# Performance work log

Hardware: AMD Instinct MI355X
Metric: run time of the kernel (lower is better)

## Reference

```python
import jax, jax.numpy as jnp
import numpy as np

KN = 2048       # 12*N spatio-temporal tokens
B = 4           # batch
D_MODEL = 512
N_HEADS = 8
HEAD_DIM = D_MODEL // N_HEADS
FACTOR = 5
U_PART = min(FACTOR * int(np.ceil(np.log(KN))), KN)  # sample_k == n_top == 40


def setup_inputs() -> dict:
    rng = jax.random.key(0)
    ks = jax.random.split(rng, 12)
    d = D_MODEL
    wscale = 1.0 / np.sqrt(d)  # xavier-ish init scale
    return {
        "query": jax.random.normal(ks[0], (KN, B, d), jnp.float32),
        "key": jax.random.normal(ks[1], (KN, B, d), jnp.float32),
        "value": jax.random.normal(ks[2], (KN, B, d), jnp.float32),
        "index_sample": jax.random.randint(ks[3], (KN, U_PART), 0, KN),
        "Wq": jax.random.normal(ks[4], (d, d), jnp.float32) * wscale,
        "bq": jnp.zeros((d,), jnp.float32),
        "Wk": jax.random.normal(ks[5], (d, d), jnp.float32) * wscale,
        "bk": jnp.zeros((d,), jnp.float32),
        "Wv": jax.random.normal(ks[6], (d, d), jnp.float32) * wscale,
        "bv": jnp.zeros((d,), jnp.float32),
        "Wo": jax.random.normal(ks[7], (d, d), jnp.float32) * wscale,
        "bo": jnp.zeros((d,), jnp.float32),
    }


def reference(query, key, value, index_sample, Wq, bq, Wk, bk, Wv, bv, Wo, bo):
    kN, Bb, d = query.shape
    H, E = N_HEADS, HEAD_DIM
    scaling = E ** -0.5

    # projections (torch Linear: x @ W.T + b); q is scaled before reshaping
    q = (query @ Wq.T + bq) * scaling
    k = key @ Wk.T + bk
    v = value @ Wv.T + bv

    # [kN, B, d] -> [B, H, kN, E]
    def to_bhne(x):
        return x.reshape(kN, Bb, H, E).transpose(1, 2, 0, 3)

    Q, K, V = to_bhne(q), to_bhne(k), to_bhne(v)

    # ProbSparse: sample U_PART keys per query row (shared index table)
    K_samp = K[:, :, index_sample, :]                       # [B,H,kN,S,E]
    QK_samp = jnp.einsum('bhne,bhnse->bhns', Q, K_samp)      # [B,H,kN,S]
    # sparsity measure M = max - mean(over full kN, as in source)
    M = QK_samp.max(axis=-1) - QK_samp.sum(axis=-1) / kN     # [B,H,kN]
    _, M_top = jax.lax.top_k(M, U_PART)                      # [B,H,S]

    # reduced queries attend over ALL keys
    Q_red = jnp.take_along_axis(Q, M_top[..., None], axis=2)  # [B,H,S,E]
    scores = jnp.einsum('bhse,bhne->bhsn', Q_red, K)          # [B,H,S,kN]
    attn = jax.nn.softmax(scores, axis=-1)
    upd = jnp.einsum('bhsn,bhne->bhse', attn, V)              # [B,H,S,E]

    # initial context = mean(V) broadcast; scatter-update the top rows
    ctx = jnp.broadcast_to(V.mean(axis=2, keepdims=True), V.shape)  # [B,H,kN,E]
    bi = jnp.arange(Bb)[:, None, None]
    hi = jnp.arange(H)[None, :, None]
    ctx = ctx.at[bi, hi, M_top].set(upd)

    out = ctx.transpose(0, 2, 1, 3).reshape(Bb, kN, d) @ Wo.T + bo  # [B,kN,d]
    return out
```

## Files before the change

kernel.cpp:

```cpp
#include <hip/hip_runtime.h>
#include <hip/hip_bf16.h>

#define KN 2048
#define BB 4
#define DM 512
#define NH 8
#define HE 64
#define UP 40
#define NBH 32
#define NROWS 8192
#define MiB(x) ((size_t)(x) << 20)

typedef __attribute__((ext_vector_type(8))) short short8;
typedef __attribute__((ext_vector_type(4))) float f32x4;

__device__ __forceinline__ ushort f2bf(float x) {
  unsigned u = __float_as_uint(x);
  unsigned r = (u + 0x7FFFu + ((u >> 16) & 1u)) >> 16;
  return (ushort)r;
}
__device__ __forceinline__ float bf2f(ushort h) {
  return __uint_as_float((unsigned)h << 16);
}

__global__ __launch_bounds__(256) void wsplit3_kernel(
    const float* __restrict__ W0, const float* __restrict__ W1,
    const float* __restrict__ W2, ushort* __restrict__ Wh,
    ushort* __restrict__ Wl) {
  const int which = blockIdx.x >> 9;
  const float* W = (which == 0) ? W0 : (which == 1) ? W1 : W2;
  size_t base = (size_t)which * 262144;
  int i = ((blockIdx.x & 511) * 256 + threadIdx.x) * 2;
  float2 v = *(const float2*)(W + i);
  ushort h0 = f2bf(v.x), h1 = f2bf(v.y);
  ushort l0 = f2bf(v.x - bf2f(h0)), l1 = f2bf(v.y - bf2f(h1));
  *(ushort2*)(Wh + base + i) = make_ushort2(h0, h1);
  *(ushort2*)(Wl + base + i) = make_ushort2(l0, l1);
}

#define APAD 40
__global__ __launch_bounds__(256) void gemm3_mfma(
    const float* __restrict__ A0, const float* __restrict__ A1,
    const float* __restrict__ A2,
    const ushort* __restrict__ Wh3, const ushort* __restrict__ Wl3,
    const float* __restrict__ bq, const float* __restrict__ bk,
    const float* __restrict__ bv, float* __restrict__ QKV) {
  __shared__ ushort AsH[128 * APAD];
  __shared__ ushort AsL[128 * APAD];
  __shared__ ushort WsH[128 * APAD];
  __shared__ ushort WsL[128 * APAD];

  const int which = blockIdx.x >> 8;
  const int local = blockIdx.x & 255;
  const int mt = (local & 7) * 8 + ((local >> 3) & 7);
  const int ot = local >> 6;
  const int m0 = mt * 128, o0 = ot * 128;

  const float* A = (which == 0) ? A0 : (which == 1) ? A1 : A2;
  const ushort* Wh = Wh3 + (size_t)which * 262144;
  const ushort* Wl = Wl3 + (size_t)which * 262144;
  const float* bias = (which == 0) ? bq : (which == 1) ? bk : bv;
  float* C = QKV + (size_t)which * 8192 * 512;
  const float scale = (which == 0) ? 0.125f : 1.0f;

  const int tid = threadIdx.x;
  const int w = tid >> 6, lane = tid & 63;
  const int wr = w >> 1, wc = w & 1;
  const int fr = lane & 15;
  const int kc = lane >> 4;

  f32x4 acc[4][4];
#pragma unroll
  for (int i = 0; i < 4; ++i)
#pragma unroll
    for (int j = 0; j < 4; ++j)
#pragma unroll
      for (int r = 0; r < 4; ++r) acc[i][j][r] = 0.f;

  const int r0 = tid >> 2, kq0 = (tid & 3) * 8;
  const int r1 = (tid + 256) >> 2, kq1 = ((tid + 256) & 3) * 8;
  const int lo0 = r0 * APAD + kq0, lo1 = r1 * APAD + kq1;

  for (int k0 = 0; k0 < 512; k0 += 32) {
#pragma unroll
    for (int i = 0; i < 4; ++i) {
      int c = tid + i * 256;
      int row = c >> 3, q = c & 7;
      float4 v = *(const float4*)(A + (size_t)(m0 + row) * 512 + k0 + q * 4);
      ushort h0 = f2bf(v.x), h1 = f2bf(v.y), h2 = f2bf(v.z), h3 = f2bf(v.w);
      ushort l0 = f2bf(v.x - bf2f(h0)), l1 = f2bf(v.y - bf2f(h1));
      ushort l2 = f2bf(v.z - bf2f(h2)), l3 = f2bf(v.w - bf2f(h3));
      *(ushort4*)(AsH + row * APAD + q * 4) = make_ushort4(h0, h1, h2, h3);
      *(ushort4*)(AsL + row * APAD + q * 4) = make_ushort4(l0, l1, l2, l3);
    }
    {
      size_t gw0 = (size_t)(o0 + r0) * 512 + k0 + kq0;
      size_t gw1 = (size_t)(o0 + r1) * 512 + k0 + kq1;
      *(short8*)(WsH + lo0) = *(const short8*)(Wh + gw0);
      *(short8*)(WsL + lo0) = *(const short8*)(Wl + gw0);
      *(short8*)(WsH + lo1) = *(const short8*)(Wh + gw1);
      *(short8*)(WsL + lo1) = *(const short8*)(Wl + gw1);
    }
    __syncthreads();

    short8 ah[4], al[4], bh[4], bl[4];
#pragma unroll
    for (int i = 0; i < 4; ++i) {
      int off = (wr * 64 + i * 16 + fr) * APAD + kc * 8;
      ah[i] = *(const short8*)(AsH + off);
      al[i] = *(const short8*)(AsL + off);
    }
#pragma unroll
    for (int j = 0; j < 4; ++j) {
      int off = (wc * 64 + j * 16 + fr) * APAD + kc * 8;
      bh[j] = *(const short8*)(WsH + off);
      bl[j] = *(const short8*)(WsL + off);
    }
#pragma unroll
    for (int i = 0; i < 4; ++i)
#pragma unroll
      for (int j = 0; j < 4; ++j) {
        acc[i][j] = __builtin_amdgcn_mfma_f32_16x16x32_bf16(
            ah[i], bh[j], acc[i][j], 0, 0, 0);
        acc[i][j] = __builtin_amdgcn_mfma_f32_16x16x32_bf16(
            ah[i], bl[j], acc[i][j], 0, 0, 0);
        acc[i][j] = __builtin_amdgcn_mfma_f32_16x16x32_bf16(
            al[i], bh[j], acc[i][j], 0, 0, 0);
      }
    __syncthreads();
  }

#pragma unroll
  for (int i = 0; i < 4; ++i)
#pragma unroll
    for (int j = 0; j < 4; ++j)
#pragma unroll
      for (int r = 0; r < 4; ++r) {
        int m = m0 + wr * 64 + i * 16 + (lane >> 4) * 4 + r;
        int o = o0 + wc * 64 + j * 16 + fr;
        C[(size_t)m * 512 + o] = (acc[i][j][r] + bias[o]) * scale;
      }
}

__global__ __launch_bounds__(256) void transposeK_kernel(
    const float* __restrict__ K, float* __restrict__ Kt) {
  const int bh = blockIdx.x & 31;
  const int nt = blockIdx.x >> 5;
  const int b = bh >> 3, h = bh & 7;
  const int n0 = nt * 128;
  const int tid = threadIdx.x;
  __shared__ float T[128][65];

#pragma unroll
  for (int i = 0; i < 8; ++i) {
    int flat = tid + i * 256;
    int r = flat >> 4;
    int c4 = flat & 15;
    float4 v = *(const float4*)(K + (((size_t)(n0 + r) * 4 + b) * 8 + h) * 64 + c4 * 4);
    T[r][c4 * 4 + 0] = v.x; T[r][c4 * 4 + 1] = v.y;
    T[r][c4 * 4 + 2] = v.z; T[r][c4 * 4 + 3] = v.w;
  }
  __syncthreads();

  const int nl = tid & 127;
  const int eg = tid >> 7;
#pragma unroll
  for (int e = eg * 32; e < eg * 32 + 32; ++e)
    Kt[((size_t)bh * 64 + e) * 2048 + n0 + nl] = T[nl][e];
}

__global__ __launch_bounds__(256) void mscore_kernel(
    const float* __restrict__ Q, const float* __restrict__ K,
    const int* __restrict__ idx, float* __restrict__ Mout) {
  const int bh = blockIdx.x & 31;
  const int c  = blockIdx.x >> 5;
  const int wv = threadIdx.x >> 6;
  const int lane = threadIdx.x & 63;
  const int n = c * 4 + wv;
  const int b = bh >> 3, h = bh & 7;
  const int g = lane >> 4;
  const int e16 = lane & 15;

  const float4 qv = *(const float4*)(Q + (((size_t)n * 4 + b) * 8 + h) * 64 + e16 * 4);

  float mx = -INFINITY, sm = 0.f;
#pragma unroll
  for (int it = 0; it < 10; ++it) {
    const int s = it * 4 + g;
    const int kn = idx[n * UP + s];
    const float4 kv = *(const float4*)(K + (((size_t)kn * 4 + b) * 8 + h) * 64 + e16 * 4);
    float d = qv.x * kv.x + qv.y * kv.y + qv.z * kv.z + qv.w * kv.w;
    d += __shfl_xor(d, 1);
    d += __shfl_xor(d, 2);
    d += __shfl_xor(d, 4);
    d += __shfl_xor(d, 8);
    mx = fmaxf(mx, d);
    sm += d;
  }
  mx = fmaxf(mx, __shfl_xor(mx, 16));
  mx = fmaxf(mx, __shfl_xor(mx, 32));
  sm += __shfl_xor(sm, 16);
  sm += __shfl_xor(sm, 32);
  if (lane == 0) Mout[(size_t)bh * 2048 + n] = mx - sm * (1.0f / (float)KN);
}

__global__ __launch_bounds__(256) void topk_kernel(
    const float* __restrict__ M, int* __restrict__ Mtop,
    int* __restrict__ flags) {
  const int bh = blockIdx.x;
  __shared__ unsigned keys[2048];
  __shared__ int hist[256];
  __shared__ int suf[256];
  __shared__ int scal[2];
  __shared__ int ties[128];
  __shared__ int cnts[2];

  const int tid = threadIdx.x;
  const int fbase = (bh >> 3) * 2048;
  const float* Mrow = M + (size_t)bh * 2048;
#pragma unroll
  for (int i = 0; i < 8; ++i) {
    int j = tid + i * 256;
    unsigned u = __float_as_uint(Mrow[j]);
    keys[j] = (u & 0x80000000u) ? ~u : (u | 0x80000000u);
  }
  if (tid < 2) cnts[tid] = 0;

  unsigned prefix = 0, prefmask = 0;
  int rank = UP;
#pragma unroll
  for (int shift = 24; shift >= 0; shift -= 8) {
    hist[tid] = 0;
    __syncthreads();
#pragma unroll
    for (int i = 0; i < 8; ++i) {
      unsigned k = keys[tid + i * 256];
      if ((k & prefmask) == prefix)
        atomicAdd(&hist[(k >> shift) & 0xFFu], 1);
    }
    __syncthreads();
    suf[tid] = hist[tid];
    __syncthreads();
#pragma unroll
    for (int off = 1; off < 256; off <<= 1) {
      int add = (tid + off < 256) ? suf[tid + off] : 0;
      __syncthreads();
      suf[tid] += add;
      __syncthreads();
    }
    {
      int above = suf[tid] - hist[tid];
      if (above < rank && rank <= suf[tid]) {
        scal[0] = tid;
        scal[1] = rank - above;
      }
    }
    __syncthreads();
    prefix |= ((unsigned)scal[0]) << shift;
    prefmask |= 0xFFu << shift;
    rank = scal[1];
    __syncthreads();
  }
  const unsigned T = prefix;

#pragma unroll
  for (int i = 0; i < 8; ++i) {
    int j = tid + i * 256;
    unsigned k = keys[j];
    if (k > T) {
      int p = atomicAdd(&cnts[0], 1);
      Mtop[bh * UP + p] = j;
      flags[fbase + j] = 1;
    } else if (k == T) {
      int p = atomicAdd(&cnts[1], 1);
      if (p < 128) ties[p] = j;
    }
  }
  __syncthreads();
  if (tid == 0) {
    int base = cnts[0];
    int need = UP - base;
    int tc = cnts[1] < 128 ? cnts[1] : 128;
    for (int s = 0; s < need; ++s) {
      int best = 1 << 30, bj = 0;
      for (int j = 0; j < tc; ++j) {
        int v = ties[j];
        if (v < best) { best = v; bj = j; }
      }
      Mtop[bh * UP + base + s] = best;
      flags[fbase + best] = 1;
      ties[bj] = 1 << 30;
    }
  }
}

__global__ __launch_bounds__(256) void meanv_part(
    const float* __restrict__ V, float* __restrict__ part) {
  const int rc = blockIdx.x >> 3;
  const int cc = blockIdx.x & 7;
  const int c = cc * 256 + threadIdx.x;
  const float* p = V + (size_t)rc * 64 * 2048 + c;
  float acc = 0.f;
#pragma unroll 8
  for (int i = 0; i < 64; ++i) acc += p[(size_t)i * 2048];
  part[(size_t)rc * 2048 + c] = acc;
}

__global__ __launch_bounds__(256) void meanv_final(
    const float* __restrict__ part, float* __restrict__ mnV) {
  const int c = blockIdx.x * 256 + threadIdx.x;
  float acc = 0.f;
#pragma unroll
  for (int r = 0; r < 32; ++r) acc += part[(size_t)r * 2048 + c];
  mnV[c] = acc * (1.0f / (float)KN);
}

__global__ void selcompact_kernel(const int* __restrict__ flags,
                                  int* __restrict__ rows,
                                  int* __restrict__ cnt) {
  const int i = blockIdx.x * 256 + threadIdx.x;
  if (flags[i]) {
    int p = atomicAdd(cnt, 1);
    rows[p] = i;
  }
}

__global__ __launch_bounds__(256) void meanout_kernel(
    const float* __restrict__ mnV, const float* __restrict__ Wo,
    const float* __restrict__ bo, float* __restrict__ mo) {
  const int b = blockIdx.x >> 3;
  const int oc = blockIdx.x & 7;
  const int ol = threadIdx.x & 63;
  const int kp = threadIdx.x >> 6;
  const int o = oc * 64 + ol;
  __shared__ float red[4][64];

  const float* m = mnV + b * 512;
  const float* w = Wo + (size_t)o * 512;
  float acc = 0.f;
#pragma unroll 8
  for (int k = kp * 128; k < kp * 128 + 128; ++k)
    acc = fmaf(m[k], w[k], acc);
  red[kp][ol] = acc;
  __syncthreads();
  if (threadIdx.x < 64) {
    float s = red[0][ol] + red[1][ol] + red[2][ol] + red[3][ol];
    mo[b * 512 + o] = s + bo[o];
  }
}

__global__ void fillout_kernel(const float* __restrict__ mo,
                               float* __restrict__ out) {
  size_t i = ((size_t)blockIdx.x * 256 + threadIdx.x) * 4;
  int d = (int)(i & 511);
  int b = (int)(i >> 20);
  float4 v = *(const float4*)(mo + (b << 9) + d);
  *(float4*)(out + i) = v;
}

__global__ __launch_bounds__(128) void fillsel_kernel(
    const float* __restrict__ mnV, const int* __restrict__ rows,
    const int* __restrict__ cnt, float* __restrict__ ctx) {
  const int bid = blockIdx.x;
  if (bid >= *cnt) return;
  const int row = rows[bid];
  const int b = row >> 11;
  float4 v = *(const float4*)(mnV + b * 512 + threadIdx.x * 4);
  *(float4*)(ctx + (size_t)row * 512 + threadIdx.x * 4) = v;
}

__global__ __launch_bounds__(256) void gemm_rows(
    const float* __restrict__ ctx, const float* __restrict__ W,
    const float* __restrict__ bias, const int* __restrict__ rows,
    const int* __restrict__ cnt, float* __restrict__ out) {
  __shared__ float As[32][36];
  __shared__ float Ws[32][68];
  __shared__ int rsel[32];
  const int rt = blockIdx.x >> 3;
  const int ot = blockIdx.x & 7;
  const int o0 = ot * 64;
  const int tid = threadIdx.x;
  const int tx = tid & 15;
  const int ty = tid >> 4;
  const int n = *cnt;

  if (rt * 32 >= n) return;

  if (tid < 32) {
    int g = rt * 32 + tid;
    rsel[tid] = (g < n) ? rows[g] : rows[0];
  }
  __syncthreads();

  float acc[2][4] = {};
  for (int k0 = 0; k0 < 512; k0 += 32) {
    {
      int row = tid >> 3, q = tid & 7;
      float4 av = *(const float4*)(ctx + (size_t)rsel[row] * 512 + k0 + q * 4);
      As[q * 4 + 0][row] = av.x; As[q * 4 + 1][row] = av.y;
      As[q * 4 + 2][row] = av.z; As[q * 4 + 3][row] = av.w;
    }
#pragma unroll
    for (int i = 0; i < 2; ++i) {
      int flat = tid + i * 256;
      int r = flat >> 3, q = flat & 7;
      float4 wv = *(const float4*)(W + (size_t)(o0 + r) * 512 + k0 + q * 4);
      Ws[q * 4 + 0][r] = wv.x; Ws[q * 4 + 1][r] = wv.y;
      Ws[q * 4 + 2][r] = wv.z; Ws[q * 4 + 3][r] = wv.w;
    }
    __syncthreads();
#pragma unroll
    for (int kk = 0; kk < 32; ++kk) {
      float a_[2], w_[4];
#pragma unroll
      for (int i = 0; i < 2; ++i) a_[i] = As[kk][ty * 2 + i];
#pragma unroll
      for (int j = 0; j < 4; ++j) w_[j] = Ws[kk][tx * 4 + j];
#pragma unroll
      for (int i = 0; i < 2; ++i)
#pragma unroll
        for (int j = 0; j < 4; ++j)
          acc[i][j] = fmaf(a_[i], w_[j], acc[i][j]);
    }
    __syncthreads();
  }

#pragma unroll
  for (int i = 0; i < 2; ++i) {
    int g = rt * 32 + ty * 2 + i;
    if (g < n) {
      int m = rsel[ty * 2 + i];
#pragma unroll
      for (int j = 0; j < 4; ++j) {
        int o = o0 + tx * 4 + j;
        out[(size_t)m * 512 + o] = acc[i][j] + bias[o];
      }
    }
  }
}

#define QG 5
#define NC 4
__global__ __launch_bounds__(256) void attn_part(
    const float* __restrict__ Q, const float* __restrict__ Kt,
    const float* __restrict__ V, const int* __restrict__ Mtop,
    float* __restrict__ pmax, float* __restrict__ psum,
    float* __restrict__ pvp) {
  const int bh = blockIdx.x & 31;
  const int t  = blockIdx.x >> 5;
  const int g  = t & 7;
  const int ch = t >> 3;
  const int b = bh >> 3, h = bh & 7;
  const int tid = threadIdx.x;
  const int wv = tid >> 6, lane = tid & 63;
  const int n0 = ch * 512;

  __shared__ float qs[QG][64];
  __shared__ float p[QG][512];
  __shared__ float redm[QG][4];
  __shared__ float reds[QG][4];
  __shared__ float pvs[4][QG][64];

  for (int i = tid; i < QG * 64; i += 256) {
    int q = i >> 6, e = i & 63;
    int nq = Mtop[bh * UP + g * QG + q];
    qs[q][e] = Q[(((size_t)nq * 4 + b) * 8 + h) * 64 + e];
  }
  __syncthreads();

  const float* ktb = Kt + (size_t)bh * 64 * 2048;
  float d0[QG] = {}, d1[QG] = {};
  const int nb = n0 + tid * 2;
  for (int e = 0; e < 64; ++e) {
    float2 kv = *(const float2*)(ktb + (size_t)e * 2048 + nb);
#pragma unroll
    for (int q = 0; q < QG; ++q) {
      float qe = qs[q][e];
      d0[q] = fmaf(qe, kv.x, d0[q]);
      d1[q] = fmaf(qe, kv.y, d1[q]);
    }
  }

#pragma unroll
  for (int q = 0; q < QG; ++q) {
    float m_ = fmaxf(d0[q], d1[q]);
#pragma unroll
    for (int off = 1; off < 64; off <<= 1)
      m_ = fmaxf(m_, __shfl_xor(m_, off));
    if (lane == 0) redm[q][wv] = m_;
  }
  __syncthreads();
  float gm[QG];
#pragma unroll
  for (int q = 0; q < QG; ++q)
    gm[q] = fmaxf(fmaxf(redm[q][0], redm[q][1]),
                  fmaxf(redm[q][2], redm[q][3]));

  float ls[QG];
#pragma unroll
  for (int q = 0; q < QG; ++q) {
    float e0 = __expf(d0[q] - gm[q]);
    float e1 = __expf(d1[q] - gm[q]);
    p[q][tid * 2] = e0;
    p[q][tid * 2 + 1] = e1;
    ls[q] = e0 + e1;
  }
#pragma unroll
  for (int q = 0; q < QG; ++q) {
    float s_ = ls[q];
#pragma unroll
    for (int off = 1; off < 64; off <<= 1)
      s_ += __shfl_xor(s_, off);
    if (lane == 0) reds[q][wv] = s_;
  }
  __syncthreads();
  float den[QG];
#pragma unroll
  for (int q = 0; q < QG; ++q)
    den[q] = reds[q][0] + reds[q][1] + reds[q][2] + reds[q][3];

  float acc[QG] = {};
  for (int nn = wv * 128; nn < wv * 128 + 128; ++nn) {
    float v = V[(((size_t)(n0 + nn) * 4 + b) * 8 + h) * 64 + lane];
#pragma unroll
    for (int q = 0; q < QG; ++q) acc[q] = fmaf(p[q][nn], v, acc[q]);
  }
#pragma unroll
  for (int q = 0; q < QG; ++q) pvs[wv][q][lane] = acc[q];
  __syncthreads();

  for (int i = tid; i < QG * 64; i += 256) {
    int q = i >> 6, e = i & 63;
    int slot = bh * UP + g * QG + q;
    float pv = pvs[0][q][e] + pvs[1][q][e] + pvs[2][q][e] + pvs[3][q][e];
    pvp[((size_t)slot * NC + ch) * 64 + e] = pv;
    if (e == 0) {
      pmax[slot * NC + ch] = gm[q];
      psum[slot * NC + ch] = den[q];
    }
  }
}

__global__ __launch_bounds__(64) void attn_combine(
    const float* __restrict__ pmax, const float* __restrict__ psum,
    const float* __restrict__ pvp, float* __restrict__ upd) {
  const int slot = blockIdx.x;
  const int e = threadIdx.x;
  float m = -INFINITY;
#pragma unroll
  for (int ch = 0; ch < NC; ++ch) m = fmaxf(m, pmax[slot * NC + ch]);
  float den = 0.f, num = 0.f;
#pragma unroll
  for (int ch = 0; ch < NC; ++ch) {
    float w = __expf(pmax[slot * NC + ch] - m);
    den = fmaf(w, psum[slot * NC + ch], den);
    num = fmaf(w, pvp[((size_t)slot * NC + ch) * 64 + e], num);
  }
  upd[(size_t)slot * 64 + e] = num / den;
}

__global__ void scatter_kernel(const float* __restrict__ upd,
                               const int* __restrict__ Mtop,
                               float* __restrict__ ctx) {
  const int blk = blockIdx.x;
  const int bh = blk / UP;
  const int b = bh >> 3, h = bh & 7;
  const int n = Mtop[blk];
  ctx[((size_t)(b * 2048 + n)) * 512 + h * 64 + threadIdx.x] =
      upd[(size_t)blk * 64 + threadIdx.x];
}

extern "C" void kernel_launch(void* const* d_in, const int* in_sizes, int n_in,
                              void* d_out, int out_size, void* d_ws,
                              size_t ws_size, hipStream_t stream) {
  const float* query = (const float*)d_in[0];
  const float* key   = (const float*)d_in[1];
  const float* value = (const float*)d_in[2];
  const int*   idxs  = (const int*)d_in[3];
  const float* Wq = (const float*)d_in[4];
  const float* bq = (const float*)d_in[5];
  const float* Wk = (const float*)d_in[6];
  const float* bk = (const float*)d_in[7];
  const float* Wv = (const float*)d_in[8];
  const float* bv = (const float*)d_in[9];
  const float* Wo = (const float*)d_in[10];
  const float* bo = (const float*)d_in[11];
  float* out = (float*)d_out;

  char* ws = (char*)d_ws;
  float*  Mbuf  = (float*)(ws + 0);
  float*  upd   = (float*)(ws + 262144);
  float*  mnV   = (float*)(ws + 589824);
  int*    Mtop  = (int*)  (ws + 598016);
  float*  vpart = (float*)(ws + 634880);
  int*    flags = (int*)  (ws + 903168);
  int*    cnt   = (int*)  (ws + 935936);
  int*    rows  = (int*)  (ws + 936192);
  float*  mo    = (float*)(ws + 941312);
  float*  QKV   = (float*)(ws + MiB(1));
  float*  Q     = QKV;
  float*  K     = (float*)(ws + MiB(17));
  float*  V     = (float*)(ws + MiB(33));
  float*  Kt    = (float*)(ws + MiB(49));
  ushort* Wh3   = (ushort*)(ws + MiB(65));
  ushort* Wl3   = (ushort*)(ws + MiB(65) + 1572864);
  float*  pmax  = (float*)(ws + MiB(68));
  float*  psum  = (float*)(ws + MiB(68) + 32768);
  float*  pvp   = (float*)(ws + MiB(68) + 65536);
  float*  ctx   = Q;

  hipMemsetAsync(flags, 0, 32768 + 4, stream);

  wsplit3_kernel<<<1536, 256, 0, stream>>>(Wq, Wk, Wv, Wh3, Wl3);
  gemm3_mfma<<<768, 256, 0, stream>>>(query, key, value, Wh3, Wl3,
                                      bq, bk, bv, QKV);

  transposeK_kernel<<<512, 256, 0, stream>>>(K, Kt);

  mscore_kernel<<<16384, 256, 0, stream>>>(Q, K, idxs, Mbuf);
  topk_kernel<<<NBH, 256, 0, stream>>>(Mbuf, Mtop, flags);
  selcompact_kernel<<<32, 256, 0, stream>>>(flags, rows, cnt);

  meanv_part<<<256, 256, 0, stream>>>(V, vpart);
  meanv_final<<<8, 256, 0, stream>>>(vpart, mnV);

  attn_part<<<NBH * 32, 256, 0, stream>>>(Q, Kt, V, Mtop, pmax, psum, pvp);
  attn_combine<<<NBH * UP, 64, 0, stream>>>(pmax, psum, pvp, upd);

  fillsel_kernel<<<NBH * UP, 128, 0, stream>>>(mnV, rows, cnt, ctx);
  scatter_kernel<<<NBH * UP, 64, 0, stream>>>(upd, Mtop, ctx);

  meanout_kernel<<<32, 256, 0, stream>>>(mnV, Wo, bo, mo);
  fillout_kernel<<<4096, 256, 0, stream>>>(mo, out);
  gemm_rows<<<320, 256, 0, stream>>>(ctx, Wo, bo, rows, cnt, out);
}
```

Before: 200.6 us.

## Retile QKV GEMM to 64x256 and drop selected-row flag compaction

The QKV projection GEMM tile changes from 128x128 to 64x256, with all four waves sharing the A rows and each wave covering a distinct 64-column slice of W. The block-to-tile mapping is also remapped by XCD. Separately, the flags memset, the flag writes in top-k and the selcompact kernel are removed; fillsel and gemm_rows now index rows directly from Mtop (1280 rows, where duplicates across heads are written redundantly with identical values). This removes a memset and a launch and changes the GEMM's A/W reuse balance, at the cost of redundant output-row writes and rows that may race, though the racing writes carry the same values.

```diff
diff --git a/kernel.cpp b/kernel.cpp
--- a/kernel.cpp
+++ b/kernel.cpp
@@ -45,16 +45,18 @@
     const ushort* __restrict__ Wh3, const ushort* __restrict__ Wl3,
     const float* __restrict__ bq, const float* __restrict__ bk,
     const float* __restrict__ bv, float* __restrict__ QKV) {
-  __shared__ ushort AsH[128 * APAD];
-  __shared__ ushort AsL[128 * APAD];
-  __shared__ ushort WsH[128 * APAD];
-  __shared__ ushort WsL[128 * APAD];
+  __shared__ ushort AsH[64 * APAD];
+  __shared__ ushort AsL[64 * APAD];
+  __shared__ ushort WsH[256 * APAD];
+  __shared__ ushort WsL[256 * APAD];
 
   const int which = blockIdx.x >> 8;
   const int local = blockIdx.x & 255;
-  const int mt = (local & 7) * 8 + ((local >> 3) & 7);
-  const int ot = local >> 6;
-  const int m0 = mt * 128, o0 = ot * 128;
+  const int xcd = local & 7;
+  const int idx = local >> 3;
+  const int ot = idx >> 4;
+  const int mt = xcd * 16 + (idx & 15);
+  const int m0 = mt * 64, o0 = ot * 256;
 
   const float* A = (which == 0) ? A0 : (which == 1) ? A1 : A2;
   const ushort* Wh = Wh3 + (size_t)which * 262144;
@@ -65,7 +67,6 @@
 
   const int tid = threadIdx.x;
   const int w = tid >> 6, lane = tid & 63;
-  const int wr = w >> 1, wc = w & 1;
   const int fr = lane & 15;
   const int kc = lane >> 4;
 
@@ -77,13 +78,9 @@
 #pragma unroll
       for (int r = 0; r < 4; ++r) acc[i][j][r] = 0.f;
 
-  const int r0 = tid >> 2, kq0 = (tid & 3) * 8;
-  const int r1 = (tid + 256) >> 2, kq1 = ((tid + 256) & 3) * 8;
-  const int lo0 = r0 * APAD + kq0, lo1 = r1 * APAD + kq1;
-
   for (int k0 = 0; k0 < 512; k0 += 32) {
 #pragma unroll
-    for (int i = 0; i < 4; ++i) {
+    for (int i = 0; i < 2; ++i) {
       int c = tid + i * 256;
       int row = c >> 3, q = c & 7;
       float4 v = *(const float4*)(A + (size_t)(m0 + row) * 512 + k0 + q * 4);
@@ -93,26 +90,27 @@
       *(ushort4*)(AsH + row * APAD + q * 4) = make_ushort4(h0, h1, h2, h3);
       *(ushort4*)(AsL + row * APAD + q * 4) = make_ushort4(l0, l1, l2, l3);
     }
-    {
-      size_t gw0 = (size_t)(o0 + r0) * 512 + k0 + kq0;
-      size_t gw1 = (size_t)(o0 + r1) * 512 + k0 + kq1;
-      *(short8*)(WsH + lo0) = *(const short8*)(Wh + gw0);
-      *(short8*)(WsL + lo0) = *(const short8*)(Wl + gw0);
-      *(short8*)(WsH + lo1) = *(const short8*)(Wh + gw1);
-      *(short8*)(WsL + lo1) = *(const short8*)(Wl + gw1);
+#pragma unroll
+    for (int i = 0; i < 4; ++i) {
+      int c = tid + i * 256;
+      int row = c >> 2, kq = (c & 3) * 8;
+      size_t gw = (size_t)(o0 + row) * 512 + k0 + kq;
+      int lo = row * APAD + kq;
+      *(short8*)(WsH + lo) = *(const short8*)(Wh + gw);
+      *(short8*)(WsL + lo) = *(const short8*)(Wl + gw);
     }
     __syncthreads();
 
     short8 ah[4], al[4], bh[4], bl[4];
 #pragma unroll
     for (int i = 0; i < 4; ++i) {
-      int off = (wr * 64 + i * 16 + fr) * APAD + kc * 8;
+      int off = (i * 16 + fr) * APAD + kc * 8;
       ah[i] = *(const short8*)(AsH + off);
       al[i] = *(const short8*)(AsL + off);
     }
 #pragma unroll
     for (int j = 0; j < 4; ++j) {
-      int off = (wc * 64 + j * 16 + fr) * APAD + kc * 8;
+      int off = (w * 64 + j * 16 + fr) * APAD + kc * 8;
       bh[j] = *(const short8*)(WsH + off);
       bl[j] = *(const short8*)(WsL + off);
     }
@@ -136,8 +134,8 @@
     for (int j = 0; j < 4; ++j)
 #pragma unroll
       for (int r = 0; r < 4; ++r) {
-        int m = m0 + wr * 64 + i * 16 + (lane >> 4) * 4 + r;
-        int o = o0 + wc * 64 + j * 16 + fr;
+        int m = m0 + i * 16 + (lane >> 4) * 4 + r;
+        int o = o0 + w * 64 + j * 16 + fr;
         C[(size_t)m * 512 + o] = (acc[i][j][r] + bias[o]) * scale;
       }
 }
@@ -205,8 +203,7 @@
 }
 
 __global__ __launch_bounds__(256) void topk_kernel(
-    const float* __restrict__ M, int* __restrict__ Mtop,
-    int* __restrict__ flags) {
+    const float* __restrict__ M, int* __restrict__ Mtop) {
   const int bh = blockIdx.x;
   __shared__ unsigned keys[2048];
   __shared__ int hist[256];
@@ -216,7 +213,6 @@
   __shared__ int cnts[2];
 
   const int tid = threadIdx.x;
-  const int fbase = (bh >> 3) * 2048;
   const float* Mrow = M + (size_t)bh * 2048;
 #pragma unroll
   for (int i = 0; i < 8; ++i) {
@@ -270,7 +266,6 @@
     if (k > T) {
       int p = atomicAdd(&cnts[0], 1);
       Mtop[bh * UP + p] = j;
-      flags[fbase + j] = 1;
     } else if (k == T) {
       int p = atomicAdd(&cnts[1], 1);
       if (p < 128) ties[p] = j;
@@ -288,7 +283,6 @@
         if (v < best) { best = v; bj = j; }
       }
       Mtop[bh * UP + base + s] = best;
-      flags[fbase + best] = 1;
       ties[bj] = 1 << 30;
     }
   }
@@ -315,16 +309,6 @@
   mnV[c] = acc * (1.0f / (float)KN);
 }
 
-__global__ void selcompact_kernel(const int* __restrict__ flags,
-                                  int* __restrict__ rows,
-                                  int* __restrict__ cnt) {
-  const int i = blockIdx.x * 256 + threadIdx.x;
-  if (flags[i]) {
-    int p = atomicAdd(cnt, 1);
-    rows[p] = i;
-  }
-}
-
 __global__ __launch_bounds__(256) void meanout_kernel(
     const float* __restrict__ mnV, const float* __restrict__ Wo,
     const float* __restrict__ bo, float* __restrict__ mo) {
@@ -359,20 +343,19 @@
 }
 
 __global__ __launch_bounds__(128) void fillsel_kernel(
-    const float* __restrict__ mnV, const int* __restrict__ rows,
-    const int* __restrict__ cnt, float* __restrict__ ctx) {
-  const int bid = blockIdx.x;
-  if (bid >= *cnt) return;
-  const int row = rows[bid];
-  const int b = row >> 11;
+    const int* __restrict__ Mtop, const float* __restrict__ mnV,
+    float* __restrict__ ctx) {
+  const int i = blockIdx.x;
+  const int b = (i / UP) >> 3;
+  const int row = b * 2048 + Mtop[i];
   float4 v = *(const float4*)(mnV + b * 512 + threadIdx.x * 4);
   *(float4*)(ctx + (size_t)row * 512 + threadIdx.x * 4) = v;
 }
 
 __global__ __launch_bounds__(256) void gemm_rows(
     const float* __restrict__ ctx, const float* __restrict__ W,
-    const float* __restrict__ bias, const int* __restrict__ rows,
-    const int* __restrict__ cnt, float* __restrict__ out) {
+    const float* __restrict__ bias, const int* __restrict__ Mtop,
+    float* __restrict__ out) {
   __shared__ float As[32][36];
   __shared__ float Ws[32][68];
   __shared__ int rsel[32];
@@ -382,13 +365,11 @@
   const int tid = threadIdx.x;
   const int tx = tid & 15;
   const int ty = tid >> 4;
-  const int n = *cnt;
-
-  if (rt * 32 >= n) return;
 
   if (tid < 32) {
     int g = rt * 32 + tid;
-    rsel[tid] = (g < n) ? rows[g] : rows[0];
+    int b = (g / UP) >> 3;
+    rsel[tid] = b * 2048 + Mtop[g];
   }
   __syncthreads();
 
@@ -427,14 +408,11 @@
 
 #pragma unroll
   for (int i = 0; i < 2; ++i) {
-    int g = rt * 32 + ty * 2 + i;
-    if (g < n) {
-      int m = rsel[ty * 2 + i];
-#pragma unroll
-      for (int j = 0; j < 4; ++j) {
-        int o = o0 + tx * 4 + j;
-        out[(size_t)m * 512 + o] = acc[i][j] + bias[o];
-      }
+    int m = rsel[ty * 2 + i];
+#pragma unroll
+    for (int j = 0; j < 4; ++j) {
+      int o = o0 + tx * 4 + j;
+      out[(size_t)m * 512 + o] = acc[i][j] + bias[o];
     }
   }
 }
@@ -593,9 +571,6 @@
   float*  mnV   = (float*)(ws + 589824);
   int*    Mtop  = (int*)  (ws + 598016);
   float*  vpart = (float*)(ws + 634880);
-  int*    flags = (int*)  (ws + 903168);
-  int*    cnt   = (int*)  (ws + 935936);
-  int*    rows  = (int*)  (ws + 936192);
   float*  mo    = (float*)(ws + 941312);
   float*  QKV   = (float*)(ws + MiB(1));
   float*  Q     = QKV;
@@ -609,8 +584,6 @@
   float*  pvp   = (float*)(ws + MiB(68) + 65536);
   float*  ctx   = Q;
 
-  hipMemsetAsync(flags, 0, 32768 + 4, stream);
-
   wsplit3_kernel<<<1536, 256, 0, stream>>>(Wq, Wk, Wv, Wh3, Wl3);
   gemm3_mfma<<<768, 256, 0, stream>>>(query, key, value, Wh3, Wl3,
                                       bq, bk, bv, QKV);
@@ -618,8 +591,7 @@
   transposeK_kernel<<<512, 256, 0, stream>>>(K, Kt);
 
   mscore_kernel<<<16384, 256, 0, stream>>>(Q, K, idxs, Mbuf);
-  topk_kernel<<<NBH, 256, 0, stream>>>(Mbuf, Mtop, flags);
-  selcompact_kernel<<<32, 256, 0, stream>>>(flags, rows, cnt);
+  topk_kernel<<<NBH, 256, 0, stream>>>(Mbuf, Mtop);
 
   meanv_part<<<256, 256, 0, stream>>>(V, vpart);
   meanv_final<<<8, 256, 0, stream>>>(vpart, mnV);
@@ -627,10 +599,10 @@
   attn_part<<<NBH * 32, 256, 0, stream>>>(Q, Kt, V, Mtop, pmax, psum, pvp);
   attn_combine<<<NBH * UP, 64, 0, stream>>>(pmax, psum, pvp, upd);
 
-  fillsel_kernel<<<NBH * UP, 128, 0, stream>>>(mnV, rows, cnt, ctx);
+  fillsel_kernel<<<NBH * UP, 128, 0, stream>>>(Mtop, mnV, ctx);
   scatter_kernel<<<NBH * UP, 64, 0, stream>>>(upd, Mtop, ctx);
 
   meanout_kernel<<<32, 256, 0, stream>>>(mnV, Wo, bo, mo);
   fillout_kernel<<<4096, 256, 0, stream>>>(mo, out);
-  gemm_rows<<<320, 256, 0, stream>>>(ctx, Wo, bo, rows, cnt, out);
-}
+  gemm_rows<<<320, 256, 0, stream>>>(ctx, Wo, bo, Mtop, out);
+}
```

Result: faster. 189.1 us (-5.7%).
